# Optimization experiments

Hardware: AMD Instinct MI355X
Metric: run time of the kernel (lower is better)

## Reference

```python
import jax, jax.numpy as jnp
import numpy as np

# AttentiveErasing hyperparameters (module defaults)
FILL = 0.0
P = 0.5
MIN_FACTOR = 0.0
MAX_FACTOR = 0.5
MIN_H = 4
MIN_W = 4

B, C, H, W = 512, 1, 224, 224


def setup_inputs() -> dict:
    key = jax.random.key(0)
    # x are attention maps in [0,1]; they are used as bernoulli probabilities.
    x = jax.random.uniform(key, (B, C, H, W), dtype=jnp.float32)
    return {"x": x}


def _per_sample_mask(xmap, factor, key):
    # xmap: [H, W] single-channel attention map for one sample
    h_dim, w_dim = xmap.shape
    k_apply, k_h, k_w = jax.random.split(key, 3)
    apply_flag = jax.random.uniform(k_apply) < P  # torch.rand(1) < p

    flat = xmap.reshape(-1)
    c = jnp.argmax(flat)                 # topk(.,1) center
    cy, cx = c // w_dim, c % w_dim
    mx = flat[c]
    mn = jnp.min(flat)
    thr = mx - (mx - mn) * factor
    prop = xmap > thr                    # proposal region

    ridx = jnp.arange(h_dim)
    cidx = jnp.arange(w_dim)
    rows = jnp.any(prop, axis=1)
    cols = jnp.any(prop, axis=0)
    any_prop = jnp.any(prop)             # empty proposals (factor==0) -> torch raises -> skip
    miny = jnp.min(jnp.where(rows, ridx, h_dim))
    maxy = jnp.max(jnp.where(rows, ridx, -1))
    minx = jnp.min(jnp.where(cols, cidx, w_dim))
    maxx = jnp.max(jnp.where(cols, cidx, -1))
    mh2 = (maxy - miny) // 2
    mw2 = (maxx - minx) // 2
    # torch.randint(min, max//2) raises when max//2 <= min -> except: pass -> skip sample
    valid = any_prop & (mh2 > MIN_H) & (mw2 > MIN_W)

    h = MIN_H + (jax.random.uniform(k_h) * jnp.maximum(mh2 - MIN_H, 1)).astype(jnp.int32)
    w = MIN_W + (jax.random.uniform(k_w) * jnp.maximum(mw2 - MIN_W, 1)).astype(jnp.int32)

    h_start = jnp.maximum(cy - h, 0)
    h_end = jnp.minimum(cy + h, w_dim)   # bug preserved: source clamps height with x.size(3)
    w_start = jnp.maximum(cx - w, 0)
    w_end = jnp.minimum(cx + w, w_dim)

    yy = ridx[:, None]
    xx = cidx[None, :]
    # keep proposal iff strictly inside window AND both coords nonzero (y*x > 0 in source)
    erase = (prop & (yy > h_start) & (yy < h_end)
             & (xx > w_start) & (xx < w_end) & (yy > 0) & (xx > 0))
    do = apply_flag & valid
    return jnp.where(do & erase, FILL, 1.0).astype(xmap.dtype)


def _forward(x):
    b = x.shape[0]
    root = jax.random.key(42)
    k_factor, k_samples, k_noise = jax.random.split(root, 3)
    factor = jax.random.uniform(k_factor, minval=MIN_FACTOR, maxval=MAX_FACTOR)
    keys = jax.random.split(k_samples, b)
    mask2d = jax.vmap(lambda xm, k: _per_sample_mask(xm, factor, k))(x[:, 0], keys)
    mask = mask2d[:, None, :, :]          # [B,1,H,W]

    inp = 0.6 * x + 0.2                   # Dropout input; values in [0.2, 0.8]
    keep_prob = jnp.clip(1.0 - jax.lax.stop_gradient(inp), 0.0, 1.0)
    prob_mask = jax.random.bernoulli(k_noise, keep_prob).astype(x.dtype)
    noise = (1.0 - mask) * prob_mask + mask  # region_mask==1 -> keep; ==0 -> bernoulli
    out = inp * noise
    return out, mask


def reference(x):
    return _forward(x)
```

## Files before the change

kernel.cpp:

```cpp
#include <hip/hip_runtime.h>
#include <cstdint>

typedef unsigned int u32;
typedef float vf4 __attribute__((ext_vector_type(4)));

#define TF_R4(a,b,r1,r2,r3,r4) \
  a += b; b = (b<<r1)|(b>>(32-r1)); b ^= a; \
  a += b; b = (b<<r2)|(b>>(32-r2)); b ^= a; \
  a += b; b = (b<<r3)|(b>>(32-r3)); b ^= a; \
  a += b; b = (b<<r4)|(b>>(32-r4)); b ^= a;

__host__ __device__ inline void tf2x32(u32 k0, u32 k1, u32& x0, u32& x1) {
  const u32 k2 = k0 ^ k1 ^ 0x1BD11BDAu;
  u32 a = x0 + k0, b = x1 + k1;
  TF_R4(a,b,13,15,26,6)   a += k1; b += k2 + 1u;
  TF_R4(a,b,17,29,16,24)  a += k2; b += k0 + 2u;
  TF_R4(a,b,13,15,26,6)   a += k0; b += k1 + 3u;
  TF_R4(a,b,17,29,16,24)  a += k1; b += k2 + 4u;
  TF_R4(a,b,13,15,26,6)   a += k2; b += k0 + 5u;
  x0 = a; x1 = b;
}

__host__ __device__ inline float u01(u32 bits) {
  union { u32 u; float f; } c; c.u = (bits >> 9) | 0x3f800000u;
  return c.f - 1.0f;
}
__host__ __device__ inline u32 rbits_scalar(u32 k0, u32 k1) {
  u32 a = 0, b = 0; tf2x32(k0, k1, a, b); return a ^ b;
}

#define BATCH   512
#define HW      224
#define S       50176
#define S4      12544
#define NTOT    25690112
#define APB     49
#define FSTR    1152

struct SP { float thr; int hs, he, wss, wee, doit; int pad0, pad1; };

__global__ __launch_bounds__(256) void k_stats(const float* __restrict__ x,
                                               float* __restrict__ fdata) {
  const int bid = blockIdx.x;
  const int b = bid >> 2, q = bid & 3;
  const int t = threadIdx.x;
  const int lane = t & 63, wv = t >> 6;
  const float* __restrict__ xs = x + (size_t)b * S;
  float* __restrict__ base = fdata + (size_t)b * FSTR;
  const bool act = lane < 56;

  vf4 cmax = (vf4){0.f, 0.f, 0.f, 0.f};
  float amax = -1.f; int aidx = 0x7fffffff; float amin = 2.f;

#pragma unroll
  for (int k = 0; k < 14; ++k) {
    const int r = q * 56 + wv * 14 + k;
    vf4 v = (vf4){-1.f, -1.f, -1.f, -1.f};
    if (act) v = ((const vf4*)(xs + (size_t)r * HW))[lane];
    float rv = fmaxf(fmaxf(v[0], v[1]), fmaxf(v[2], v[3]));
    if (act) {
      cmax[0] = fmaxf(cmax[0], v[0]); cmax[1] = fmaxf(cmax[1], v[1]);
      cmax[2] = fmaxf(cmax[2], v[2]); cmax[3] = fmaxf(cmax[3], v[3]);
      const int fb = r * HW + lane * 4;
      if (v[0] > amax) { amax = v[0]; aidx = fb; }
      if (v[1] > amax) { amax = v[1]; aidx = fb + 1; }
      if (v[2] > amax) { amax = v[2]; aidx = fb + 2; }
      if (v[3] > amax) { amax = v[3]; aidx = fb + 3; }
      amin = fminf(amin, fminf(fminf(v[0], v[1]), fminf(v[2], v[3])));
    }
    for (int off = 32; off; off >>= 1) rv = fmaxf(rv, __shfl_xor(rv, off));
    if (lane == 0) base[r] = rv;
  }
  for (int off = 32; off; off >>= 1) {
    float v2 = __shfl_xor(amax, off);
    int   i2 = __shfl_xor(aidx, off);
    float n2 = __shfl_xor(amin, off);
    if (v2 > amax || (v2 == amax && i2 < aidx)) { amax = v2; aidx = i2; }
    amin = fminf(amin, n2);
  }
  __shared__ vf4 cmw[4][56];
  __shared__ float wmx[4]; __shared__ int wix[4]; __shared__ float wmn[4];
  if (act) cmw[wv][lane] = cmax;
  if (lane == 0) { wmx[wv] = amax; wix[wv] = aidx; wmn[wv] = amin; }
  __syncthreads();
  if (t < 56) {
    vf4 a = cmw[0][t], c1 = cmw[1][t], c2 = cmw[2][t], c3 = cmw[3][t];
    vf4 m;
    m[0] = fmaxf(fmaxf(a[0], c1[0]), fmaxf(c2[0], c3[0]));
    m[1] = fmaxf(fmaxf(a[1], c1[1]), fmaxf(c2[1], c3[1]));
    m[2] = fmaxf(fmaxf(a[2], c1[2]), fmaxf(c2[2], c3[2]));
    m[3] = fmaxf(fmaxf(a[3], c1[3]), fmaxf(c2[3], c3[3]));
    ((vf4*)(base + 224 + q * 224))[t] = m;
  }
  if (t == 0) {
    float mx = wmx[0]; int ix = wix[0]; float mn = wmn[0];
    for (int wI = 1; wI < 4; ++wI) {
      if (wmx[wI] > mx || (wmx[wI] == mx && wix[wI] < ix)) { mx = wmx[wI]; ix = wix[wI]; }
      mn = fminf(mn, wmn[wI]);
    }
    base[1120 + q * 3 + 0] = mx;
    base[1120 + q * 3 + 1] = __int_as_float(ix);
    base[1120 + q * 3 + 2] = mn;
  }
}

__global__ __launch_bounds__(256) void k_box(const float* __restrict__ fdata,
                                             SP* __restrict__ sp,
                                             float factor, u32 ks0, u32 ks1) {
  const int b = blockIdx.x;
  const int t = threadIdx.x;
  const int lane = t & 63, wv = t >> 6;
  const float* __restrict__ base = fdata + (size_t)b * FSTR;

  float mx = -1.f; int ix = 0x7fffffff; float mn = 2.f;
#pragma unroll
  for (int q = 0; q < 4; ++q) {
    const float v = base[1120 + q * 3 + 0];
    const int   i = __float_as_int(base[1120 + q * 3 + 1]);
    const float n = base[1120 + q * 3 + 2];
    if (v > mx || (v == mx && i < ix)) { mx = v; ix = i; }
    mn = fminf(mn, n);
  }
  const float thr = __fsub_rn(mx, __fmul_rn(__fsub_rn(mx, mn), factor));

  u32 kb0 = 0, kb1 = (u32)b; tf2x32(ks0, ks1, kb0, kb1);
  u32 ka0 = 0, ka1 = 0; tf2x32(kb0, kb1, ka0, ka1);
  const bool apply = u01(rbits_scalar(ka0, ka1)) < 0.5f;
  if (!apply) {
    if (t == 0) {
      SP p; p.thr = thr; p.hs = 0; p.he = 0; p.wss = 0; p.wee = 0;
      p.doit = 0; p.pad0 = 0; p.pad1 = 0;
      sp[b] = p;
    }
    return;
  }

  int miny = HW, maxy = -1, minx = HW, maxx = -1;
  if (t < HW) {
    if (base[t] > thr) { miny = t; maxy = t; }
    const float c0 = base[224 + t],       c1 = base[224 + 224 + t];
    const float c2 = base[224 + 448 + t], c3 = base[224 + 672 + t];
    if (fmaxf(fmaxf(c0, c1), fmaxf(c2, c3)) > thr) { minx = t; maxx = t; }
  }
  for (int off = 32; off; off >>= 1) {
    miny = min(miny, __shfl_xor(miny, off));
    maxy = max(maxy, __shfl_xor(maxy, off));
    minx = min(minx, __shfl_xor(minx, off));
    maxx = max(maxx, __shfl_xor(maxx, off));
  }
  __shared__ int r0[4], r1[4], r2[4], r3[4];
  if (lane == 0) { r0[wv] = miny; r1[wv] = maxy; r2[wv] = minx; r3[wv] = maxx; }
  __syncthreads();
  if (t == 0) {
    int mny = r0[0], mxy = r1[0], mnx = r2[0], mxx = r3[0];
    for (int wI = 1; wI < 4; ++wI) {
      mny = min(mny, r0[wI]); mxy = max(mxy, r1[wI]);
      mnx = min(mnx, r2[wI]); mxx = max(mxx, r3[wI]);
    }
    const bool any = (mxy >= 0);
    const int mh2 = (mxy - mny) / 2;
    const int mw2 = (mxx - mnx) / 2;
    const bool valid = any && (mh2 > 4) && (mw2 > 4);

    u32 kh0 = 0, kh1 = 1; tf2x32(kb0, kb1, kh0, kh1);
    u32 kw0 = 0, kw1 = 2; tf2x32(kb0, kb1, kw0, kw1);
    const float uh = u01(rbits_scalar(kh0, kh1));
    const float uw = u01(rbits_scalar(kw0, kw1));

    const int cy = ix / HW, cx = ix % HW;
    const int h = 4 + (int)(uh * (float)max(mh2 - 4, 1));
    const int w = 4 + (int)(uw * (float)max(mw2 - 4, 1));
    SP p;
    p.thr = thr;
    p.hs = max(cy - h, 0); p.he = min(cy + h, HW);
    p.wss = max(cx - w, 0); p.wee = min(cx + w, HW);
    p.doit = valid ? 1 : 0;
    p.pad0 = 0; p.pad1 = 0;
    sp[b] = p;
  }
}

__global__ __launch_bounds__(256) void k_apply(const float* __restrict__ x,
                                               const SP* __restrict__ sp,
                                               float* __restrict__ out,
                                               u32 kn0, u32 kn1) {
  const int bid = blockIdx.x;
  const int b   = bid / APB;
  const int i   = (bid % APB) * 256 + threadIdx.x;
  const SP p = sp[b];
  const vf4 vv = ((const vf4*)(x + (size_t)b * S))[i];
  vf4* __restrict__ os = (vf4*)(out + (size_t)b * S);
  vf4* __restrict__ ms = (vf4*)(out + (size_t)NTOT + (size_t)b * S);

  const int base = i * 4;
  const int y = base / HW, x0 = base % HW;
  const bool yin = p.doit && (y > p.hs) && (y < p.he) && (y > 0);
  const u32 eoff = (u32)b * (u32)S;

  vf4 o, m;
  int need = 0;
#pragma unroll
  for (int j = 0; j < 4; ++j) {
    const float val = vv[j];
    const float inp = __fadd_rn(__fmul_rn(0.6f, val), 0.2f);
    const int xx = x0 + j;
    const bool mz = yin && (val > p.thr) && (xx > p.wss) && (xx < p.wee) && (xx > 0);
    m[j] = mz ? 0.0f : 1.0f;
    o[j] = inp;
    if (mz) need |= 1 << j;
  }
  if (need) {
#pragma unroll
    for (int j = 0; j < 4; ++j) {
      if (need & (1 << j)) {
        const float kp = fminf(fmaxf(__fsub_rn(1.0f, o[j]), 0.0f), 1.0f);
        u32 c0 = 0u, c1 = eoff + (u32)(base + j);
        tf2x32(kn0, kn1, c0, c1);
        if (!(u01(c0 ^ c1) < kp)) o[j] = 0.0f;
      }
    }
  }
  __builtin_nontemporal_store(o, &os[i]);
  __builtin_nontemporal_store(m, &ms[i]);
}

extern "C" void kernel_launch(void* const* d_in, const int* in_sizes, int n_in,
                              void* d_out, int out_size, void* d_ws, size_t ws_size,
                              hipStream_t stream) {
  const float* x = (const float*)d_in[0];
  float* out = (float*)d_out;
  SP*    sp    = (SP*)d_ws;
  float* fdata = (float*)((char*)d_ws + 16384);

  u32 kf0 = 0, kf1 = 0; tf2x32(0u, 42u, kf0, kf1);
  u32 ks0 = 0, ks1 = 1; tf2x32(0u, 42u, ks0, ks1);
  u32 kn0 = 0, kn1 = 2; tf2x32(0u, 42u, kn0, kn1);
  float factor = fmaxf(0.0f, u01(rbits_scalar(kf0, kf1)) * 0.5f);

  hipLaunchKernelGGL(k_stats, dim3(BATCH * 4), dim3(256), 0, stream, x, fdata);
  hipLaunchKernelGGL(k_box,   dim3(BATCH), dim3(256), 0, stream,
                     fdata, sp, factor, ks0, ks1);
  hipLaunchKernelGGL(k_apply, dim3(BATCH * APB), dim3(256), 0, stream,
                     x, sp, out, kn0, kn1);
}
```

Measured before the change: 72.83 us.

## Write default outputs during stats pass and patch only erased box region

The stats kernel now also writes the default output (0.6x+0.2) and an all-ones mask while it reads x. This removes the separate full pass that re-read x and wrote both outputs. The box kernel and apply kernel are merged into a k_fix kernel. It recomputes the box per sample and, only for samples that apply, rewrites the pixels inside the window that pass the threshold with the Bernoulli-masked value and a zero mask. The cost is scattered scalar reads and writes in the fix pass, plus redundant box computation across the 8 blocks per sample.

Measured after the change: 93.17 us. 1.28x slower.

```diff
diff --git a/kernel.cpp b/kernel.cpp
--- a/kernel.cpp
+++ b/kernel.cpp
@@ -32,22 +32,24 @@
 #define BATCH   512
 #define HW      224
 #define S       50176
-#define S4      12544
 #define NTOT    25690112
-#define APB     49
 #define FSTR    1152
-
-struct SP { float thr; int hs, he, wss, wee, doit; int pad0, pad1; };
+#define FIXPB   8
+
 
 __global__ __launch_bounds__(256) void k_stats(const float* __restrict__ x,
+                                               float* __restrict__ out,
                                                float* __restrict__ fdata) {
   const int bid = blockIdx.x;
   const int b = bid >> 2, q = bid & 3;
   const int t = threadIdx.x;
   const int lane = t & 63, wv = t >> 6;
   const float* __restrict__ xs = x + (size_t)b * S;
+  float* __restrict__ os = out + (size_t)b * S;
+  float* __restrict__ ms = out + (size_t)NTOT + (size_t)b * S;
   float* __restrict__ base = fdata + (size_t)b * FSTR;
   const bool act = lane < 56;
+  const vf4 ones = (vf4){1.f, 1.f, 1.f, 1.f};
 
   vf4 cmax = (vf4){0.f, 0.f, 0.f, 0.f};
   float amax = -1.f; int aidx = 0x7fffffff; float amin = 2.f;
@@ -59,6 +61,13 @@
     if (act) v = ((const vf4*)(xs + (size_t)r * HW))[lane];
     float rv = fmaxf(fmaxf(v[0], v[1]), fmaxf(v[2], v[3]));
     if (act) {
+      vf4 o;
+      o[0] = __fadd_rn(__fmul_rn(0.6f, v[0]), 0.2f);
+      o[1] = __fadd_rn(__fmul_rn(0.6f, v[1]), 0.2f);
+      o[2] = __fadd_rn(__fmul_rn(0.6f, v[2]), 0.2f);
+      o[3] = __fadd_rn(__fmul_rn(0.6f, v[3]), 0.2f);
+      __builtin_nontemporal_store(o,    &((vf4*)(os + (size_t)r * HW))[lane]);
+      __builtin_nontemporal_store(ones, &((vf4*)(ms + (size_t)r * HW))[lane]);
       cmax[0] = fmaxf(cmax[0], v[0]); cmax[1] = fmaxf(cmax[1], v[1]);
       cmax[2] = fmaxf(cmax[2], v[2]); cmax[3] = fmaxf(cmax[3], v[3]);
       const int fb = r * HW + lane * 4;
@@ -104,52 +113,65 @@
   }
 }
 
-__global__ __launch_bounds__(256) void k_box(const float* __restrict__ fdata,
-                                             SP* __restrict__ sp,
-                                             float factor, u32 ks0, u32 ks1) {
-  const int b = blockIdx.x;
+__global__ __launch_bounds__(256) void k_fix(const float* __restrict__ x,
+                                             float* __restrict__ out,
+                                             const float* __restrict__ fdata,
+                                             float factor,
+                                             u32 ks0, u32 ks1,
+                                             u32 kn0, u32 kn1) {
+  const int bid = blockIdx.x;
+  const int b = bid >> 3, qq = bid & 7;
   const int t = threadIdx.x;
   const int lane = t & 63, wv = t >> 6;
-  const float* __restrict__ base = fdata + (size_t)b * FSTR;
-
-  float mx = -1.f; int ix = 0x7fffffff; float mn = 2.f;
-#pragma unroll
-  for (int q = 0; q < 4; ++q) {
-    const float v = base[1120 + q * 3 + 0];
-    const int   i = __float_as_int(base[1120 + q * 3 + 1]);
-    const float n = base[1120 + q * 3 + 2];
-    if (v > mx || (v == mx && i < ix)) { mx = v; ix = i; }
-    mn = fminf(mn, n);
-  }
-  const float thr = __fsub_rn(mx, __fmul_rn(__fsub_rn(mx, mn), factor));
 
   u32 kb0 = 0, kb1 = (u32)b; tf2x32(ks0, ks1, kb0, kb1);
   u32 ka0 = 0, ka1 = 0; tf2x32(kb0, kb1, ka0, ka1);
-  const bool apply = u01(rbits_scalar(ka0, ka1)) < 0.5f;
-  if (!apply) {
-    if (t == 0) {
-      SP p; p.thr = thr; p.hs = 0; p.he = 0; p.wss = 0; p.wee = 0;
-      p.doit = 0; p.pad0 = 0; p.pad1 = 0;
-      sp[b] = p;
-    }
-    return;
-  }
-
-  int miny = HW, maxy = -1, minx = HW, maxx = -1;
-  if (t < HW) {
-    if (base[t] > thr) { miny = t; maxy = t; }
-    const float c0 = base[224 + t],       c1 = base[224 + 224 + t];
-    const float c2 = base[224 + 448 + t], c3 = base[224 + 672 + t];
-    if (fmaxf(fmaxf(c0, c1), fmaxf(c2, c3)) > thr) { minx = t; maxx = t; }
-  }
-  for (int off = 32; off; off >>= 1) {
-    miny = min(miny, __shfl_xor(miny, off));
-    maxy = max(maxy, __shfl_xor(maxy, off));
-    minx = min(minx, __shfl_xor(minx, off));
-    maxx = max(maxx, __shfl_xor(maxx, off));
-  }
+  if (!(u01(rbits_scalar(ka0, ka1)) < 0.5f)) return;
+
+  const float* __restrict__ base = fdata + (size_t)b * FSTR;
+  __shared__ float rm[224], cmx[224];
+  __shared__ float sc_thr; __shared__ int sc_ix;
   __shared__ int r0[4], r1[4], r2[4], r3[4];
-  if (lane == 0) { r0[wv] = miny; r1[wv] = maxy; r2[wv] = minx; r3[wv] = maxx; }
+  __shared__ int sbox[5];
+
+  if (t < 224) {
+    rm[t] = base[t];
+    float c = base[224 + t];
+    c = fmaxf(c, base[224 + 224 + t]);
+    c = fmaxf(c, base[224 + 448 + t]);
+    c = fmaxf(c, base[224 + 672 + t]);
+    cmx[t] = c;
+  }
+  if (t == 0) {
+    float mx = -1.f; int ix = 0x7fffffff; float mn = 2.f;
+#pragma unroll
+    for (int q2 = 0; q2 < 4; ++q2) {
+      const float v = base[1120 + q2 * 3 + 0];
+      const int   i = __float_as_int(base[1120 + q2 * 3 + 1]);
+      const float n = base[1120 + q2 * 3 + 2];
+      if (v > mx || (v == mx && i < ix)) { mx = v; ix = i; }
+      mn = fminf(mn, n);
+    }
+    sc_thr = __fsub_rn(mx, __fmul_rn(__fsub_rn(mx, mn), factor));
+    sc_ix = ix;
+  }
+  __syncthreads();
+  const float thr = sc_thr;
+
+  {
+    int miny = HW, maxy = -1, minx = HW, maxx = -1;
+    if (t < HW) {
+      if (rm[t] > thr)  { miny = t; maxy = t; }
+      if (cmx[t] > thr) { minx = t; maxx = t; }
+    }
+    for (int off = 32; off; off >>= 1) {
+      miny = min(miny, __shfl_xor(miny, off));
+      maxy = max(maxy, __shfl_xor(maxy, off));
+      minx = min(minx, __shfl_xor(minx, off));
+      maxx = max(maxx, __shfl_xor(maxx, off));
+    }
+    if (lane == 0) { r0[wv] = miny; r1[wv] = maxy; r2[wv] = minx; r3[wv] = maxx; }
+  }
   __syncthreads();
   if (t == 0) {
     int mny = r0[0], mxy = r1[0], mnx = r2[0], mxx = r3[0];
@@ -166,62 +188,37 @@
     u32 kw0 = 0, kw1 = 2; tf2x32(kb0, kb1, kw0, kw1);
     const float uh = u01(rbits_scalar(kh0, kh1));
     const float uw = u01(rbits_scalar(kw0, kw1));
-
-    const int cy = ix / HW, cx = ix % HW;
+    const int cy = sc_ix / HW, cx = sc_ix % HW;
     const int h = 4 + (int)(uh * (float)max(mh2 - 4, 1));
     const int w = 4 + (int)(uw * (float)max(mw2 - 4, 1));
-    SP p;
-    p.thr = thr;
-    p.hs = max(cy - h, 0); p.he = min(cy + h, HW);
-    p.wss = max(cx - w, 0); p.wee = min(cx + w, HW);
-    p.doit = valid ? 1 : 0;
-    p.pad0 = 0; p.pad1 = 0;
-    sp[b] = p;
-  }
-}
-
-__global__ __launch_bounds__(256) void k_apply(const float* __restrict__ x,
-                                               const SP* __restrict__ sp,
-                                               float* __restrict__ out,
-                                               u32 kn0, u32 kn1) {
-  const int bid = blockIdx.x;
-  const int b   = bid / APB;
-  const int i   = (bid % APB) * 256 + threadIdx.x;
-  const SP p = sp[b];
-  const vf4 vv = ((const vf4*)(x + (size_t)b * S))[i];
-  vf4* __restrict__ os = (vf4*)(out + (size_t)b * S);
-  vf4* __restrict__ ms = (vf4*)(out + (size_t)NTOT + (size_t)b * S);
-
-  const int base = i * 4;
-  const int y = base / HW, x0 = base % HW;
-  const bool yin = p.doit && (y > p.hs) && (y < p.he) && (y > 0);
-  const u32 eoff = (u32)b * (u32)S;
-
-  vf4 o, m;
-  int need = 0;
-#pragma unroll
-  for (int j = 0; j < 4; ++j) {
-    const float val = vv[j];
-    const float inp = __fadd_rn(__fmul_rn(0.6f, val), 0.2f);
-    const int xx = x0 + j;
-    const bool mz = yin && (val > p.thr) && (xx > p.wss) && (xx < p.wee) && (xx > 0);
-    m[j] = mz ? 0.0f : 1.0f;
-    o[j] = inp;
-    if (mz) need |= 1 << j;
-  }
-  if (need) {
-#pragma unroll
-    for (int j = 0; j < 4; ++j) {
-      if (need & (1 << j)) {
-        const float kp = fminf(fmaxf(__fsub_rn(1.0f, o[j]), 0.0f), 1.0f);
-        u32 c0 = 0u, c1 = eoff + (u32)(base + j);
+    sbox[0] = max(cy - h, 0); sbox[1] = min(cy + h, HW);
+    sbox[2] = max(cx - w, 0); sbox[3] = min(cx + w, HW);
+    sbox[4] = valid ? 1 : 0;
+  }
+  __syncthreads();
+  if (!sbox[4]) return;
+  const int hs = sbox[0], he = sbox[1], wss = sbox[2], wee = sbox[3];
+
+  const int xx = wss + 1 + t;
+  const bool cin = (xx < wee);
+  const float* __restrict__ xs = x + (size_t)b * S;
+  float* __restrict__ os = out + (size_t)b * S;
+  float* __restrict__ ms = out + (size_t)NTOT + (size_t)b * S;
+
+  for (int y = hs + 1 + qq; y < he; y += FIXPB) {
+    if (cin) {
+      const int pix = y * HW + xx;
+      const float val = xs[pix];
+      if (val > thr) {
+        const float inp = __fadd_rn(__fmul_rn(0.6f, val), 0.2f);
+        const float kp  = fminf(fmaxf(__fsub_rn(1.0f, inp), 0.0f), 1.0f);
+        u32 c0 = 0u, c1 = (u32)b * (u32)S + (u32)pix;
         tf2x32(kn0, kn1, c0, c1);
-        if (!(u01(c0 ^ c1) < kp)) o[j] = 0.0f;
+        os[pix] = (u01(c0 ^ c1) < kp) ? inp : 0.0f;
+        ms[pix] = 0.0f;
       }
     }
   }
-  __builtin_nontemporal_store(o, &os[i]);
-  __builtin_nontemporal_store(m, &ms[i]);
 }
 
 extern "C" void kernel_launch(void* const* d_in, const int* in_sizes, int n_in,
@@ -229,17 +226,15 @@
                               hipStream_t stream) {
   const float* x = (const float*)d_in[0];
   float* out = (float*)d_out;
-  SP*    sp    = (SP*)d_ws;
-  float* fdata = (float*)((char*)d_ws + 16384);
+  float* fdata = (float*)d_ws;
 
   u32 kf0 = 0, kf1 = 0; tf2x32(0u, 42u, kf0, kf1);
   u32 ks0 = 0, ks1 = 1; tf2x32(0u, 42u, ks0, ks1);
   u32 kn0 = 0, kn1 = 2; tf2x32(0u, 42u, kn0, kn1);
   float factor = fmaxf(0.0f, u01(rbits_scalar(kf0, kf1)) * 0.5f);
 
-  hipLaunchKernelGGL(k_stats, dim3(BATCH * 4), dim3(256), 0, stream, x, fdata);
-  hipLaunchKernelGGL(k_box,   dim3(BATCH), dim3(256), 0, stream,
-                     fdata, sp, factor, ks0, ks1);
-  hipLaunchKernelGGL(k_apply, dim3(BATCH * APB), dim3(256), 0, stream,
-                     x, sp, out, kn0, kn1);
-}
+  hipLaunchKernelGGL(k_stats, dim3(BATCH * 4), dim3(256), 0, stream,
+                     x, out, fdata);
+  hipLaunchKernelGGL(k_fix, dim3(BATCH * FIXPB), dim3(256), 0, stream,
+                     x, out, fdata, factor, ks0, ks1, kn0, kn1);
+}
```
